# Performance work log

Measured on AMD Instinct MI355X. Metric: run time of the kernel, lower is better.

The kernel has to match this reference:

```python
import jax, jax.numpy as jnp
import numpy as np
from jax import lax

S, B, C = 128, 32, 16
VW, VC = 100000, 100
DW, DC = 256, 64
HW, HC = 512, 128
T = 17


def setup_inputs():
    key = jax.random.key(0)
    it = iter(jax.random.split(key, 40))

    def p(shape, scale=0.05):
        return jax.random.normal(next(it), shape, jnp.float32) * scale

    inp = {}
    inp['sentence'] = jax.random.randint(next(it), (S, B), 2, VW)
    inp['char'] = jax.random.randint(next(it), (B, S, C), 2, VC)
    inp['tags'] = jax.random.randint(next(it), (S, B), 0, T)
    inp['W_we'] = p((VW, DW)).at[1].set(0.0)  # padding_idx=1 row zeroed
    inp['W_ce'] = p((VC, DC)).at[1].set(0.0)
    Hc2, Hw2 = HC // 2, HW // 2
    for d in ('f', 'b'):
        inp['c_Wih_' + d] = p((4 * Hc2, DC))
        inp['c_Whh_' + d] = p((4 * Hc2, Hc2))
        inp['c_b_' + d] = p((4 * Hc2,))
        inp['w_Wih_' + d] = p((4 * Hw2, DW + HC))
        inp['w_Whh_' + d] = p((4 * Hw2, Hw2))
        inp['w_b_' + d] = p((4 * Hw2,))
    inp['emit_W'] = p((T, HW))
    inp['emit_b'] = p((T,))
    inp['crf_trans'] = p((T, T), 0.1)
    inp['crf_start'] = p((T,), 0.1)
    inp['crf_end'] = p((T,), 0.1)
    return inp


def _lstm(xs, Wih, Whh, b):
    # xs: (L, N, D); torch gate order i,f,g,o
    H = Whh.shape[1]

    def step(carry, x):
        h, c = carry
        g = x @ Wih.T + h @ Whh.T + b
        i, f, gg, o = jnp.split(g, 4, axis=-1)
        c = jax.nn.sigmoid(f) * c + jax.nn.sigmoid(i) * jnp.tanh(gg)
        h = jax.nn.sigmoid(o) * jnp.tanh(c)
        return (h, c), h

    z = jnp.zeros((xs.shape[1], H), xs.dtype)
    (hT, _), hs = lax.scan(step, (z, z), xs)
    return hs, hT


def _bilstm(xs, Wf, Uf, bf, Wb, Ub, bb):
    hs_f, hT_f = _lstm(xs, Wf, Uf, bf)
    hs_b, hT_b = _lstm(xs[::-1], Wb, Ub, bb)
    return jnp.concatenate([hs_f, hs_b[::-1]], axis=-1), hT_f, hT_b


def _crf_nll(em, tags, mask, trans, start, end):
    # em: (S,B,T); pytorch-crf log-likelihood, reduction='sum'; returns -llh
    b_idx = jnp.arange(em.shape[1])
    mf = mask.astype(em.dtype)
    score0 = start[tags[0]] + em[0, b_idx, tags[0]]

    def num_step(carry, inp):
        s, prev = carry
        e_t, t_t, m_t = inp
        s = s + (trans[prev, t_t] + e_t[b_idx, t_t]) * m_t
        prev = jnp.where(m_t > 0, t_t, prev)
        return (s, prev), None

    (num, last), _ = lax.scan(num_step, (score0, tags[0]), (em[1:], tags[1:], mf[1:]))
    num = num + end[last]

    alpha0 = start[None, :] + em[0]

    def den_step(alpha, inp):
        e_t, m_t = inp
        nxt = jax.scipy.special.logsumexp(alpha[:, :, None] + trans[None] + e_t[:, None, :], axis=1)
        return jnp.where(m_t[:, None] > 0, nxt, alpha), None

    alpha, _ = lax.scan(den_step, alpha0, (em[1:], mf[1:]))
    den = jax.scipy.special.logsumexp(alpha + end[None, :], axis=1)
    return -jnp.sum(num - den)


def reference(sentence, char, tags, W_we, W_ce, c_Wih_f, c_Whh_f, c_b_f, c_Wih_b, c_Whh_b, c_b_b, w_Wih_f, w_Whh_f, w_b_f, w_Wih_b, w_Whh_b, w_b_b, emit_W, emit_b, crf_trans, crf_start, crf_end):
    # char features: batch the per-position char BiLSTM across (B*S)
    ce = W_ce[char]  # (B,S,C,DC)
    ce = jnp.transpose(ce, (2, 0, 1, 3)).reshape(C, B * S, DC)
    _, hTf, hTb = _bilstm(ce, c_Wih_f, c_Whh_f, c_b_f, c_Wih_b, c_Whh_b, c_b_b)
    ch = jnp.concatenate([hTf, hTb], axis=-1).reshape(B, S, HC).transpose(1, 0, 2)  # (S,B,HC)
    x = jnp.concatenate([ch, W_we[sentence]], axis=-1)  # (S,B,HC+DW)
    out, _, _ = _bilstm(x, w_Wih_f, w_Whh_f, w_b_f, w_Wih_b, w_Whh_b, w_b_b)  # (S,B,HW)
    em = out @ emit_W.T + emit_b  # (S,B,T)
    mask = sentence != 1
    return _crf_nll(em, tags, mask, crf_trans, crf_start, crf_end)
```

## Files before the change

### kernel.cpp

```cpp
#include <hip/hip_runtime.h>
#include <math.h>

#define SS 128
#define BB 32
#define CC 16
#define DW 256
#define DC 64
#define HC 128
#define KX 384
#define TT 17

typedef __attribute__((ext_vector_type(8))) short bf16x8;
typedef __attribute__((ext_vector_type(4))) float f32x4;
typedef unsigned long long ull_t;

__device__ __forceinline__ float sigf(float x) { return 1.0f / (1.0f + __expf(-x)); }
__device__ __forceinline__ float tanhfast(float x) {
  float xc = fminf(fmaxf(x, -15.f), 15.f);
  float e = __expf(2.f * xc);
  return (e - 1.f) / (e + 1.f);
}
__device__ __forceinline__ unsigned short f2bf(float x) {
  unsigned int u = __float_as_uint(x);
  u += 0x7FFF + ((u >> 16) & 1);
  return (unsigned short)(u >> 16);
}
__device__ __forceinline__ unsigned ld_u32(const unsigned* p) {
  return __hip_atomic_load(p, __ATOMIC_RELAXED, __HIP_MEMORY_SCOPE_AGENT);
}
__device__ __forceinline__ void st_u32(unsigned* p, unsigned v) {
  __hip_atomic_store(p, v, __ATOMIC_RELAXED, __HIP_MEMORY_SCOPE_AGENT);
}
__device__ __forceinline__ ull_t ld_ull(const ull_t* p) {
  return __hip_atomic_load(p, __ATOMIC_RELAXED, __HIP_MEMORY_SCOPE_AGENT);
}
__device__ __forceinline__ void st_ull(ull_t* p, ull_t v) {
  __hip_atomic_store(p, v, __ATOMIC_RELAXED, __HIP_MEMORY_SCOPE_AGENT);
}

__global__ __launch_bounds__(256) void k0_ihvocab(
    const float* __restrict__ Wce,
    const float* __restrict__ WihF, const float* __restrict__ bF,
    const float* __restrict__ WihB, const float* __restrict__ bB,
    float* __restrict__ ihv) {
  int blk = blockIdx.x;
  int d = blk / 100, v = blk % 100;
  const float* Wih = d ? WihB : WihF;
  const float* bb  = d ? bB   : bF;
  __shared__ float ce[DC];
  if (threadIdx.x < DC) ce[threadIdx.x] = Wce[v * DC + threadIdx.x];
  __syncthreads();
  int g = threadIdx.x;
  float acc = bb[g];
  #pragma unroll 16
  for (int k = 0; k < DC; ++k) acc += ce[k] * Wih[g * DC + k];
  ihv[(d * 100 + v) * 256 + g] = acc;
}

__global__ __launch_bounds__(256) void k1_char(
    const int* __restrict__ charidx,
    const float* __restrict__ WhhF, const float* __restrict__ WhhB,
    const float* __restrict__ ihv,
    float* __restrict__ x)
{
  int blk = blockIdx.x;
  int d = blk >> 8;
  int n0 = (blk & 255) * 16;
  const float* Whh = d ? WhhB : WhhF;

  __shared__ float Wl[256 * 64];
  __shared__ float hl[16 * 68];

  for (int i = threadIdx.x; i < 256 * 64; i += 256) {
    int g = i >> 6, k = i & 63;
    Wl[g * 64 + (((k >> 2) ^ (g & 15)) << 2) + (k & 3)] = Whh[i];
  }
  __syncthreads();

  int hh = threadIdx.x & 63;
  int ng = threadIdx.x >> 6;
  float c[4] = {0.f, 0.f, 0.f, 0.f};
  float h[4] = {0.f, 0.f, 0.f, 0.f};
  int bb_[4], ss_[4];
  #pragma unroll
  for (int m = 0; m < 4; ++m) {
    int n = n0 + ng + 4 * m;
    bb_[m] = n >> 7; ss_[m] = n & 127;
  }

  for (int t = 0; t < CC; ++t) {
    int cpos = d ? (CC - 1 - t) : t;
    float acc[4][4];
    #pragma unroll
    for (int m = 0; m < 4; ++m) {
      int v = charidx[bb_[m] * (SS * CC) + ss_[m] * CC + cpos];
      const float* base = ihv + (d * 100 + v) * 256 + hh;
      acc[m][0] = base[0]; acc[m][1] = base[64]; acc[m][2] = base[128]; acc[m][3] = base[192];
    }
    if (t > 0) {
      #pragma unroll 4
      for (int k = 0; k < 64; k += 4) {
        int kc = k >> 2;
        float4 w4[4];
        #pragma unroll
        for (int q = 0; q < 4; ++q)
          w4[q] = *(const float4*)&Wl[(q * 64 + hh) * 64 + ((kc ^ (hh & 15)) << 2)];
        #pragma unroll
        for (int m = 0; m < 4; ++m) {
          float4 h4 = *(const float4*)&hl[(ng + 4 * m) * 68 + k];
          #pragma unroll
          for (int q = 0; q < 4; ++q)
            acc[m][q] += h4.x * w4[q].x + h4.y * w4[q].y + h4.z * w4[q].z + h4.w * w4[q].w;
        }
      }
      __syncthreads();
    }
    #pragma unroll
    for (int m = 0; m < 4; ++m) {
      float ig = sigf(acc[m][0]);
      float fg = sigf(acc[m][1]);
      float gg = tanhfast(acc[m][2]);
      float og = sigf(acc[m][3]);
      c[m] = fg * c[m] + ig * gg;
      h[m] = og * tanhfast(c[m]);
      hl[(ng + 4 * m) * 68 + hh] = h[m];
    }
    __syncthreads();
  }
  #pragma unroll
  for (int m = 0; m < 4; ++m) {
    int row = ss_[m] * BB + bb_[m];
    x[row * KX + d * 64 + hh] = h[m];
  }
}

__global__ __launch_bounds__(64) void k2_we(
    const int* __restrict__ sentence, const float* __restrict__ Wwe,
    float* __restrict__ x) {
  int row = blockIdx.x;
  int idx = sentence[row];
  const float4* src = (const float4*)(Wwe + (size_t)idx * DW);
  float4* dst = (float4*)(x + (size_t)row * KX + HC);
  dst[threadIdx.x] = src[threadIdx.x];
}

__global__ __launch_bounds__(256) void kcv(
    const float* __restrict__ x,
    const float* __restrict__ WihF, const float* __restrict__ WihB,
    unsigned short* __restrict__ xb, unsigned short* __restrict__ wb) {
  int i = blockIdx.x * 256 + threadIdx.x;
  const float* src; unsigned short* dst; int off;
  if (i < 196608)      { src = x;    dst = xb;              off = i; }
  else if (i < 245760) { src = WihF; dst = wb;              off = i - 196608; }
  else                 { src = WihB; dst = wb + 1024 * 384; off = i - 245760; }
  float4 a = *(const float4*)(src + (size_t)off * 8);
  float4 b = *(const float4*)(src + (size_t)off * 8 + 4);
  bf16x8 o;
  o[0] = (short)f2bf(a.x); o[1] = (short)f2bf(a.y);
  o[2] = (short)f2bf(a.z); o[3] = (short)f2bf(a.w);
  o[4] = (short)f2bf(b.x); o[5] = (short)f2bf(b.y);
  o[6] = (short)f2bf(b.z); o[7] = (short)f2bf(b.w);
  *(bf16x8*)(dst + (size_t)off * 8) = o;
}

__global__ __launch_bounds__(256) void k3m(
    const unsigned short* __restrict__ xb, const unsigned short* __restrict__ wb,
    const float* __restrict__ bF, const float* __restrict__ bB,
    float* __restrict__ wg) {
  const int n0 = blockIdx.x * 128;
  const int m0 = blockIdx.y * 128;
  const int d  = n0 >> 10;
  const int gb0 = n0 & 1023;
  const float* bias = d ? bB : bF;

  __shared__ unsigned short Ab[128 * 40];
  __shared__ unsigned short Bb[128 * 40];

  const int tid = threadIdx.x;
  const int l = tid & 63, w = tid >> 6;
  const int wm = w >> 1, wn = w & 1;
  const int l15 = l & 15, q4 = l >> 4;
  const int sr = tid >> 1, shf = tid & 1;

  f32x4 acc[4][4];
  #pragma unroll
  for (int mr = 0; mr < 4; ++mr)
    #pragma unroll
    for (int nr = 0; nr < 4; ++nr)
      acc[mr][nr] = (f32x4){0.f, 0.f, 0.f, 0.f};

  for (int kt = 0; kt < 12; ++kt) {
    __syncthreads();
    {
      const bf16x8* sA = (const bf16x8*)(xb + (size_t)(m0 + sr) * KX + kt * 32 + shf * 16);
      const bf16x8* sB = (const bf16x8*)(wb + (size_t)(n0 + sr) * KX + kt * 32 + shf * 16);
      bf16x8 a0 = sA[0], a1 = sA[1];
      bf16x8 b0 = sB[0], b1 = sB[1];
      *(bf16x8*)&Ab[sr * 40 + shf * 16]     = a0;
      *(bf16x8*)&Ab[sr * 40 + shf * 16 + 8] = a1;
      *(bf16x8*)&Bb[sr * 40 + shf * 16]     = b0;
      *(bf16x8*)&Bb[sr * 40 + shf * 16 + 8] = b1;
    }
    __syncthreads();
    bf16x8 Afr[4], Bfr[4];
    #pragma unroll
    for (int mr = 0; mr < 4; ++mr)
      Afr[mr] = *(const bf16x8*)&Ab[(wm * 64 + mr * 16 + l15) * 40 + q4 * 8];
    #pragma unroll
    for (int nr = 0; nr < 4; ++nr)
      Bfr[nr] = *(const bf16x8*)&Bb[(wn * 64 + nr * 16 + l15) * 40 + q4 * 8];
    #pragma unroll
    for (int mr = 0; mr < 4; ++mr)
      #pragma unroll
      for (int nr = 0; nr < 4; ++nr)
        acc[mr][nr] = __builtin_amdgcn_mfma_f32_16x16x32_bf16(Afr[mr], Bfr[nr], acc[mr][nr], 0, 0, 0);
  }

  #pragma unroll
  for (int nr = 0; nr < 4; ++nr) {
    int gcol = gb0 + wn * 64 + nr * 16 + l15;
    float bv = bias[gcol];
    #pragma unroll
    for (int mr = 0; mr < 4; ++mr) {
      int mrow = m0 + wm * 64 + mr * 16 + q4 * 4;
      float* dst = wg + ((size_t)(d * 4096 + mrow)) * 1024 + gcol;
      #pragma unroll
      for (int r = 0; r < 4; ++r)
        dst[(size_t)r * 1024] = acc[mr][nr][r] + bv;
    }
  }
}

__global__ __launch_bounds__(64, 1) void k4_word(
    const float* __restrict__ WhhF, const float* __restrict__ WhhB,
    const float* __restrict__ wg,
    float* __restrict__ outh,
    unsigned short* __restrict__ hbuf,
    unsigned int* __restrict__ flags) {
  const int blk = blockIdx.x;
  const int d = blk >> 4, widx = blk & 15;
  const int l = threadIdx.x;
  const int l15 = l & 15, q4 = l >> 4;
  const int j0w = widx * 16;
  const float* __restrict__ Whh = d ? WhhB : WhhF;
  unsigned short* hb_d = hbuf + d * 16384;
  unsigned int* fl = flags + d * 16;

  __shared__ unsigned short hl[32 * 24];

  bf16x8 Bf[4][8];
  #pragma unroll
  for (int q = 0; q < 4; ++q) {
    const float* wr = Whh + (size_t)(q * 256 + j0w + l15) * 256 + q4 * 8;
    #pragma unroll
    for (int ks = 0; ks < 8; ++ks) {
      float4 lo = *(const float4*)(wr + ks * 32);
      float4 hi = *(const float4*)(wr + ks * 32 + 4);
      bf16x8 f;
      f[0] = (short)f2bf(lo.x); f[1] = (short)f2bf(lo.y);
      f[2] = (short)f2bf(lo.z); f[3] = (short)f2bf(lo.w);
      f[4] = (short)f2bf(hi.x); f[5] = (short)f2bf(hi.y);
      f[6] = (short)f2bf(hi.z); f[7] = (short)f2bf(hi.w);
      Bf[q][ks] = f;
    }
  }

  float cst[8];
  #pragma unroll
  for (int i = 0; i < 8; ++i) cst[i] = 0.f;

  const int rb = l >> 1;
  const int rh = l & 1;

  for (int t = 0; t < SS; ++t) {
    const int s = d ? (SS - 1 - t) : t;

    f32x4 acc[4][2];
    const float* wgs = wg + ((size_t)d * 4096 + (size_t)s * 32) * 1024 + j0w + l15;
    #pragma unroll
    for (int q = 0; q < 4; ++q)
      #pragma unroll
      for (int mt = 0; mt < 2; ++mt)
        #pragma unroll
        for (int r = 0; r < 4; ++r)
          acc[q][mt][r] = wgs[(size_t)(q4 * 4 + r + mt * 16) * 1024 + q * 256];

    if (t > 0) {
      for (;;) {
        unsigned tg = ld_u32(fl + l15);
        if (__all((int)(tg >= (unsigned)t))) break;
        __builtin_amdgcn_s_sleep(1);
      }

      const unsigned short* hp = hb_d + ((t - 1) & 1) * 8192 + q4 * 8;
      bf16x8 Af[2][8];
      #pragma unroll
      for (int mt = 0; mt < 2; ++mt)
        #pragma unroll
        for (int ks = 0; ks < 8; ++ks) {
          const ull_t* p = (const ull_t*)(hp + (size_t)(l15 + mt * 16) * 256 + ks * 32);
          union { ull_t u[2]; bf16x8 v; } cvt;
          cvt.u[0] = ld_ull(p);
          cvt.u[1] = ld_ull(p + 1);
          Af[mt][ks] = cvt.v;
        }
      #pragma unroll
      for (int q = 0; q < 4; ++q)
        #pragma unroll
        for (int mt = 0; mt < 2; ++mt) {
          f32x4 c = acc[q][mt];
          #pragma unroll
          for (int ks = 0; ks < 8; ++ks)
            c = __builtin_amdgcn_mfma_f32_16x16x32_bf16(Af[mt][ks], Bf[q][ks], c, 0, 0, 0);
          acc[q][mt] = c;
        }
    }

    float hv[8];
    #pragma unroll
    for (int mt = 0; mt < 2; ++mt)
      #pragma unroll
      for (int r = 0; r < 4; ++r) {
        int ix = mt * 4 + r;
        float ig = sigf(acc[0][mt][r]);
        float fg = sigf(acc[1][mt][r]);
        float gg = tanhfast(acc[2][mt][r]);
        float og = sigf(acc[3][mt][r]);
        float c2 = fg * cst[ix] + ig * gg;
        cst[ix] = c2;
        hv[ix] = og * tanhfast(c2);
      }

    #pragma unroll
    for (int mt = 0; mt < 2; ++mt)
      #pragma unroll
      for (int r = 0; r < 4; ++r)
        hl[(q4 * 4 + r + mt * 16) * 24 + l15] = f2bf(hv[mt * 4 + r]);
    ull_t plo = *(const ull_t*)&hl[rb * 24 + rh * 8];
    ull_t phi = *(const ull_t*)&hl[rb * 24 + rh * 8 + 4];
    ull_t* dst = (ull_t*)(hb_d + (t & 1) * 8192 + (size_t)rb * 256 + j0w + rh * 8);
    st_ull(dst, plo);
    st_ull(dst + 1, phi);
    asm volatile("s_waitcnt vmcnt(0)" ::: "memory");
    if (l == 0) st_u32(fl + widx, (unsigned)(t + 1));

    float* op = outh + (size_t)(s * 32) * 512 + d * 256 + j0w + l15;
    #pragma unroll
    for (int mt = 0; mt < 2; ++mt)
      #pragma unroll
      for (int r = 0; r < 4; ++r)
        __builtin_nontemporal_store(hv[mt * 4 + r], op + (size_t)(q4 * 4 + r + mt * 16) * 512);
  }
}

__global__ __launch_bounds__(64) void k5_emit(
    const float* __restrict__ outh, const float* __restrict__ eW,
    const float* __restrict__ eb, float* __restrict__ em) {
  int row = blockIdx.x;
  int t = threadIdx.x;
  if (t < TT) {
    const float4* o4 = (const float4*)(outh + (size_t)row * 512);
    const float4* w4 = (const float4*)(eW + (size_t)t * 512);
    float acc = 0.f;
    #pragma unroll 16
    for (int k = 0; k < 128; ++k) {
      float4 a = o4[k], bq = w4[k];
      acc += a.x * bq.x + a.y * bq.y + a.z * bq.z + a.w * bq.w;
    }
    em[row * TT + t] = acc + eb[t];
  }
}

__global__ __launch_bounds__(64) void k6_crf(
    const int* __restrict__ sentence, const int* __restrict__ tags,
    const float* __restrict__ em, const float* __restrict__ trans,
    const float* __restrict__ startv, const float* __restrict__ endv,
    float* __restrict__ outp) {
  int b = blockIdx.x;
  int j = threadIdx.x;
  __shared__ float ash[TT];
  __shared__ float red[TT];
  float tc[TT];
  float alpha = 0.f;
  if (j < TT) {
    #pragma unroll
    for (int i = 0; i < TT; ++i) tc[i] = trans[i * TT + j];
    alpha = startv[j] + em[(0 * BB + b) * TT + j];
  }
  for (int s = 1; s < SS; ++s) {
    if (j < TT) ash[j] = alpha;
    __syncthreads();
    int m = (sentence[s * BB + b] != 1) ? 1 : 0;
    if (j < TT) {
      float mx = -1e30f;
      #pragma unroll
      for (int i = 0; i < TT; ++i) mx = fmaxf(mx, ash[i] + tc[i]);
      float sum = 0.f;
      #pragma unroll
      for (int i = 0; i < TT; ++i) sum += __expf(ash[i] + tc[i] - mx);
      float nxt = mx + __logf(sum) + em[(s * BB + b) * TT + j];
      if (m) alpha = nxt;
    }
    __syncthreads();
  }
  if (j < TT) red[j] = alpha + endv[j];
  __syncthreads();
  if (j == 0) {
    float mx = -1e30f;
    for (int i = 0; i < TT; ++i) mx = fmaxf(mx, red[i]);
    float sum = 0.f;
    for (int i = 0; i < TT; ++i) sum += __expf(red[i] - mx);
    float den = mx + __logf(sum);
    int prev = tags[0 * BB + b];
    float num = startv[prev] + em[(0 * BB + b) * TT + prev];
    for (int s = 1; s < SS; ++s) {
      int tg = tags[s * BB + b];
      if (sentence[s * BB + b] != 1) {
        num += trans[prev * TT + tg] + em[(s * BB + b) * TT + tg];
        prev = tg;
      }
    }
    num += endv[prev];
    atomicAdd(outp, den - num);
  }
}

extern "C" void kernel_launch(void* const* d_in, const int* in_sizes, int n_in,
                              void* d_out, int out_size, void* d_ws, size_t ws_size,
                              hipStream_t stream) {
  (void)in_sizes; (void)n_in; (void)out_size; (void)ws_size;
  const int*   sentence = (const int*)d_in[0];
  const int*   charidx  = (const int*)d_in[1];
  const int*   tags     = (const int*)d_in[2];
  const float* Wwe   = (const float*)d_in[3];
  const float* Wce   = (const float*)d_in[4];
  const float* cWihF = (const float*)d_in[5];
  const float* cWhhF = (const float*)d_in[6];
  const float* cbF   = (const float*)d_in[7];
  const float* wWihF = (const float*)d_in[8];
  const float* wWhhF = (const float*)d_in[9];
  const float* wbF   = (const float*)d_in[10];
  const float* cWihB = (const float*)d_in[11];
  const float* cWhhB = (const float*)d_in[12];
  const float* cbB   = (const float*)d_in[13];
  const float* wWihB = (const float*)d_in[14];
  const float* wWhhB = (const float*)d_in[15];
  const float* wbB   = (const float*)d_in[16];
  const float* eW    = (const float*)d_in[17];
  const float* eb    = (const float*)d_in[18];
  const float* trans = (const float*)d_in[19];
  const float* startv= (const float*)d_in[20];
  const float* endv  = (const float*)d_in[21];

  char* ws = (char*)d_ws;
  unsigned int*   flags = (unsigned int*)(ws + 0);
  float*          ihv   = (float*)(ws + 512);
  float*          x     = (float*)(ws + 205312);
  float*          wg    = (float*)(ws + 6496768);
  unsigned short* hbuf  = (unsigned short*)(ws + 40051200);
  float*          outh  = (float*)(ws + 40116736);
  float*          em    = (float*)(ws + 48505344);
  unsigned short* xb = (unsigned short*)(ws + 40116736);
  unsigned short* wb = (unsigned short*)(ws + 40116736 + 3145728);

  hipMemsetAsync(flags, 0, 512, stream);
  hipMemsetAsync(d_out, 0, sizeof(float), stream);

  k0_ihvocab<<<200, 256, 0, stream>>>(Wce, cWihF, cbF, cWihB, cbB, ihv);
  k1_char<<<512, 256, 0, stream>>>(charidx, cWhhF, cWhhB, ihv, x);
  k2_we<<<4096, 64, 0, stream>>>(sentence, Wwe, x);
  kcv<<<1152, 256, 0, stream>>>(x, wWihF, wWihB, xb, wb);
  k3m<<<dim3(16, 32), 256, 0, stream>>>(xb, wb, wbF, wbB, wg);
  k4_word<<<32, 64, 0, stream>>>(wWhhF, wWhhB, wg, outh, hbuf, flags);
  k5_emit<<<4096, 64, 0, stream>>>(outh, eW, eb, em);
  k6_crf<<<32, 64, 0, stream>>>(sentence, tags, em, trans, startv, endv, (float*)d_out);
}
```

Baseline: 954.9 us.

## Write bf16 activations directly from producers, stage emit rows in LDS, parallelize CRF numerator

The char LSTM and word-embedding kernels now write bf16 values straight into the GEMM input buffer. This removes the fp32 staging buffer and its conversion pass, and the conversion kernel now only handles the weights. The emission kernel loads each output row into shared memory cooperatively before the dot products. The CRF kernel computes the gold-path numerator on a spare thread, overlapped with the forward recursion, instead of running it serially afterwards on thread 0. Together these aim to cut memory traffic and serial tail work, at the cost of extra packing logic and reliance on xb not aliasing other live buffers.

```diff
diff --git a/kernel.cpp b/kernel.cpp
--- a/kernel.cpp
+++ b/kernel.cpp
@@ -61,7 +61,7 @@
     const int* __restrict__ charidx,
     const float* __restrict__ WhhF, const float* __restrict__ WhhB,
     const float* __restrict__ ihv,
-    float* __restrict__ x)
+    unsigned short* __restrict__ xb)
 {
   int blk = blockIdx.x;
   int d = blk >> 8;
@@ -130,29 +130,28 @@
   #pragma unroll
   for (int m = 0; m < 4; ++m) {
     int row = ss_[m] * BB + bb_[m];
-    x[row * KX + d * 64 + hh] = h[m];
+    xb[(size_t)row * KX + d * 64 + hh] = f2bf(h[m]);
   }
 }
 
 __global__ __launch_bounds__(64) void k2_we(
     const int* __restrict__ sentence, const float* __restrict__ Wwe,
-    float* __restrict__ x) {
+    unsigned short* __restrict__ xb) {
   int row = blockIdx.x;
   int idx = sentence[row];
-  const float4* src = (const float4*)(Wwe + (size_t)idx * DW);
-  float4* dst = (float4*)(x + (size_t)row * KX + HC);
-  dst[threadIdx.x] = src[threadIdx.x];
+  float4 v = ((const float4*)(Wwe + (size_t)idx * DW))[threadIdx.x];
+  ull_t p = (ull_t)f2bf(v.x) | ((ull_t)f2bf(v.y) << 16) |
+            ((ull_t)f2bf(v.z) << 32) | ((ull_t)f2bf(v.w) << 48);
+  *(ull_t*)(xb + (size_t)row * KX + HC + threadIdx.x * 4) = p;
 }
 
 __global__ __launch_bounds__(256) void kcv(
-    const float* __restrict__ x,
     const float* __restrict__ WihF, const float* __restrict__ WihB,
-    unsigned short* __restrict__ xb, unsigned short* __restrict__ wb) {
+    unsigned short* __restrict__ wb) {
   int i = blockIdx.x * 256 + threadIdx.x;
   const float* src; unsigned short* dst; int off;
-  if (i < 196608)      { src = x;    dst = xb;              off = i; }
-  else if (i < 245760) { src = WihF; dst = wb;              off = i - 196608; }
-  else                 { src = WihB; dst = wb + 1024 * 384; off = i - 245760; }
+  if (i < 49152) { src = WihF; dst = wb;              off = i; }
+  else           { src = WihB; dst = wb + 1024 * 384; off = i - 49152; }
   float4 a = *(const float4*)(src + (size_t)off * 8);
   float4 b = *(const float4*)(src + (size_t)off * 8 + 4);
   bf16x8 o;
@@ -357,17 +356,22 @@
     const float* __restrict__ outh, const float* __restrict__ eW,
     const float* __restrict__ eb, float* __restrict__ em) {
   int row = blockIdx.x;
-  int t = threadIdx.x;
-  if (t < TT) {
-    const float4* o4 = (const float4*)(outh + (size_t)row * 512);
-    const float4* w4 = (const float4*)(eW + (size_t)t * 512);
+  int tid = threadIdx.x;
+  __shared__ float osh[512];
+  const float4* src = (const float4*)(outh + (size_t)row * 512);
+  ((float4*)osh)[tid]      = src[tid];
+  ((float4*)osh)[tid + 64] = src[tid + 64];
+  __syncthreads();
+  if (tid < TT) {
+    const float4* o4 = (const float4*)osh;
+    const float4* w4 = (const float4*)(eW + (size_t)tid * 512);
     float acc = 0.f;
     #pragma unroll 16
     for (int k = 0; k < 128; ++k) {
       float4 a = o4[k], bq = w4[k];
       acc += a.x * bq.x + a.y * bq.y + a.z * bq.z + a.w * bq.w;
     }
-    em[row * TT + t] = acc + eb[t];
+    em[row * TT + tid] = acc + eb[tid];
   }
 }
 
@@ -380,12 +384,17 @@
   int j = threadIdx.x;
   __shared__ float ash[TT];
   __shared__ float red[TT];
+  __shared__ float numsh;
   float tc[TT];
   float alpha = 0.f;
+  float num = 0.f; int prev = 0;
   if (j < TT) {
     #pragma unroll
     for (int i = 0; i < TT; ++i) tc[i] = trans[i * TT + j];
     alpha = startv[j] + em[(0 * BB + b) * TT + j];
+  } else if (j == TT) {
+    prev = tags[0 * BB + b];
+    num = startv[prev] + em[(0 * BB + b) * TT + prev];
   }
   for (int s = 1; s < SS; ++s) {
     if (j < TT) ash[j] = alpha;
@@ -400,10 +409,15 @@
       for (int i = 0; i < TT; ++i) sum += __expf(ash[i] + tc[i] - mx);
       float nxt = mx + __logf(sum) + em[(s * BB + b) * TT + j];
       if (m) alpha = nxt;
+    } else if (j == TT && m) {
+      int tg = tags[s * BB + b];
+      num += trans[prev * TT + tg] + em[(s * BB + b) * TT + tg];
+      prev = tg;
     }
     __syncthreads();
   }
   if (j < TT) red[j] = alpha + endv[j];
+  if (j == TT) numsh = num + endv[prev];
   __syncthreads();
   if (j == 0) {
     float mx = -1e30f;
@@ -411,17 +425,7 @@
     float sum = 0.f;
     for (int i = 0; i < TT; ++i) sum += __expf(red[i] - mx);
     float den = mx + __logf(sum);
-    int prev = tags[0 * BB + b];
-    float num = startv[prev] + em[(0 * BB + b) * TT + prev];
-    for (int s = 1; s < SS; ++s) {
-      int tg = tags[s * BB + b];
-      if (sentence[s * BB + b] != 1) {
-        num += trans[prev * TT + tg] + em[(s * BB + b) * TT + tg];
-        prev = tg;
-      }
-    }
-    num += endv[prev];
-    atomicAdd(outp, den - num);
+    atomicAdd(outp, den - numsh);
   }
 }
 
@@ -455,7 +459,6 @@
   char* ws = (char*)d_ws;
   unsigned int*   flags = (unsigned int*)(ws + 0);
   float*          ihv   = (float*)(ws + 512);
-  float*          x     = (float*)(ws + 205312);
   float*          wg    = (float*)(ws + 6496768);
   unsigned short* hbuf  = (unsigned short*)(ws + 40051200);
   float*          outh  = (float*)(ws + 40116736);
@@ -467,9 +470,9 @@
   hipMemsetAsync(d_out, 0, sizeof(float), stream);
 
   k0_ihvocab<<<200, 256, 0, stream>>>(Wce, cWihF, cbF, cWihB, cbB, ihv);
-  k1_char<<<512, 256, 0, stream>>>(charidx, cWhhF, cWhhB, ihv, x);
-  k2_we<<<4096, 64, 0, stream>>>(sentence, Wwe, x);
-  kcv<<<1152, 256, 0, stream>>>(x, wWihF, wWihB, xb, wb);
+  k1_char<<<512, 256, 0, stream>>>(charidx, cWhhF, cWhhB, ihv, xb);
+  k2_we<<<4096, 64, 0, stream>>>(sentence, Wwe, xb);
+  kcv<<<384, 256, 0, stream>>>(wWihF, wWihB, wb);
   k3m<<<dim3(16, 32), 256, 0, stream>>>(xb, wb, wbF, wbB, wg);
   k4_word<<<32, 64, 0, stream>>>(wWhhF, wWhhB, wg, outh, hbuf, flags);
   k5_emit<<<4096, 64, 0, stream>>>(outh, eW, eb, em);
```

New measurement: 967.1 us. Within noise of the previous version (+1.3%).
